# Optimization experiments

Hardware: AMD Instinct MI355X
Metric: run time of the kernel (lower is better)

The kernel has to match this reference:

```python
import jax, jax.numpy as jnp
import numpy as np
from jax import lax

SCORE_THR = 0.1
IOU_THR = 0.3
NUM_CLASSES = 80
MAX_COORD = 4096.0  # class offset for class-aware NMS (boxes live in [0, ~1100])


def setup_inputs() -> dict:
    key = jax.random.key(0)
    bs, n = 4, 4096
    k1, k2, k3, k4 = jax.random.split(key, 4)
    # realistic boxes: centers in [0,1024], w/h in [10,210]
    cxcy = jax.random.uniform(k1, (bs, n, 2), minval=0.0, maxval=1024.0)
    wh = jax.random.uniform(k2, (bs, n, 2), minval=10.0, maxval=210.0)
    x1y1 = cxcy - wh * 0.5
    x2y2 = cxcy + wh * 0.5
    scores = jax.random.uniform(k3, (bs, n, 1), minval=0.0, maxval=1.0)
    cls = jax.random.randint(k4, (bs, n, 1), 0, NUM_CLASSES).astype(jnp.float32)
    batch_preds = jnp.concatenate([x1y1, x2y2, scores, cls], axis=-1)  # [bs, n, 6]
    return {"batch_preds": batch_preds}


def _iou_matrix(boxes):
    # boxes: [N, 4] (x1, y1, x2, y2) -> pairwise IoU [N, N]
    x1, y1, x2, y2 = boxes[:, 0], boxes[:, 1], boxes[:, 2], boxes[:, 3]
    area = (x2 - x1) * (y2 - y1)
    ix1 = jnp.maximum(x1[:, None], x1[None, :])
    iy1 = jnp.maximum(y1[:, None], y1[None, :])
    ix2 = jnp.minimum(x2[:, None], x2[None, :])
    iy2 = jnp.minimum(y2[:, None], y2[None, :])
    inter = jnp.maximum(ix2 - ix1, 0.0) * jnp.maximum(iy2 - iy1, 0.0)
    return inter / (area[:, None] + area[None, :] - inter + 1e-9)


def _nms_image(preds):
    # preds: [N, 6]. Returns preds zeroed where not kept (fixed-shape mask NMS).
    n = preds.shape[0]
    boxes, scores, cls = preds[:, :4], preds[:, 4], preds[:, 5]
    valid = scores >= SCORE_THR
    # class-aware trick == per-class NMS: offset boxes by class so cross-class IoU = 0
    obox = boxes + (cls * MAX_COORD)[:, None]
    order = jnp.argsort(-jnp.where(valid, scores, -jnp.inf))
    sboxes = obox[order]
    svalid = valid[order]
    iou = _iou_matrix(sboxes)  # [N, N]
    idxs = jnp.arange(n)

    def body(suppressed, inp):
        iou_row, v_i, i = inp
        keep_i = v_i & jnp.logical_not(suppressed[i])
        suppressed = suppressed | (keep_i & (iou_row > IOU_THR) & (idxs > i))
        return suppressed, keep_i

    _, keep_sorted = lax.scan(body, jnp.zeros((n,), bool), (iou, svalid, idxs))
    keep = jnp.zeros((n,), bool).at[order].set(keep_sorted)
    return preds * keep[:, None].astype(preds.dtype)


def reference(batch_preds):
    # Fixed-shape formulation of score filtering + per-class greedy NMS:
    # suppressed / below-threshold rows are zeroed instead of removed.
    return jax.vmap(_nms_image)(batch_preds)
```

## Files before the change

kernel.cpp:

```cpp
#include <hip/hip_runtime.h>
#include <hip/hip_bf16.h>

typedef unsigned long long u64;

#define BS 4
#define NBOX 4096
#define NCLS 80
#define CAPC 128
#define ZBLK 16
#define SCORE_THR 0.1f
#define IOU_THR 0.3f
#define MAX_COORD 4096.0f

__global__ __launch_bounds__(64) void k_nms_all(const float* __restrict__ preds,
                                                float* __restrict__ out) {
    const int img = blockIdx.y;
    const int bx = blockIdx.x;
    const int lane = threadIdx.x;
    const float* P = preds + (size_t)img * NBOX * 6;
    float* O = out + (size_t)img * NBOX * 6;

    if (bx >= NCLS) {
        const int base = (bx - NCLS) * (NBOX / ZBLK);
#pragma unroll
        for (int r = 0; r < (NBOX / ZBLK) / 64; ++r) {
            int e = base + lane + r * 64;
            float sc = P[(size_t)e * 6 + 4];
            if (sc < SCORE_THR) {
                float* W = O + (size_t)e * 6;
#pragma unroll
                for (int q = 0; q < 6; ++q) W[q] = 0.0f;
            }
        }
        return;
    }

    __shared__ unsigned mem[CAPC];
    __shared__ unsigned scnt;
    __shared__ u64 skey[CAPC];
    __shared__ float4 sbx[CAPC];
    __shared__ unsigned sidx[CAPC];
    const int cls = bx;
    if (lane == 0) scnt = 0;
    __syncthreads();

    for (int m = lane; m < NBOX; m += 64) {
        float2 sc = *(const float2*)(P + (size_t)m * 6 + 4);
        if (sc.x >= SCORE_THR && (int)sc.y == cls) {
            unsigned slot = atomicAdd(&scnt, 1u);
            if (slot < CAPC) mem[slot] = (unsigned)m;
        }
    }
    __syncthreads();
    const int s = (int)min(scnt, (unsigned)CAPC);
    if (s == 0) return;

    u64 key[2];
    float4 bx2[2] = {make_float4(0,0,0,0), make_float4(0,0,0,0)};
    unsigned oi[2] = {0, 0};
#pragma unroll
    for (int r = 0; r < 2; ++r) {
        int m = lane + 64 * r;
        key[r] = ~0ull;
        if (m < s) {
            unsigned e = mem[m];
            oi[r] = e;
            const float* R = P + (size_t)e * 6;
            float x1 = R[0], y1 = R[1], x2 = R[2], y2 = R[3], sc = R[4], cl = R[5];
            float off = cl * MAX_COORD;
            bx2[r] = make_float4(x1 + off, y1 + off, x2 + off, y2 + off);
            unsigned u = __float_as_uint(sc);
            u = (u & 0x80000000u) ? ~u : (u | 0x80000000u);
            key[r] = ((u64)(~u) << 32) | (u64)e;
        }
        skey[m] = key[r];
    }
    __syncthreads();

    int rank[2] = {0, 0};
    for (int j = 0; j < s; ++j) {
        u64 kj = skey[j];
        rank[0] += (kj < key[0]);
        rank[1] += (kj < key[1]);
    }
    __syncthreads();
#pragma unroll
    for (int r = 0; r < 2; ++r) {
        int m = lane + 64 * r;
        if (m < s) { sbx[rank[r]] = bx2[r]; sidx[rank[r]] = oi[r]; }
    }
    __syncthreads();

    float4 cb[2] = {make_float4(0,0,0,0), make_float4(0,0,0,0)};
    float ca[2] = {0.f, 0.f};
    unsigned coi[2] = {0, 0};
    bool removed[2];
#pragma unroll
    for (int r = 0; r < 2; ++r) {
        int c = lane + 64 * r;
        removed[r] = (c >= s);
        if (c < s) {
            cb[r] = sbx[c];
            coi[r] = sidx[c];
            ca[r] = (cb[r].z - cb[r].x) * (cb[r].w - cb[r].y);
        }
    }

    for (int i = 0; i < s; ++i) {
        u64 mA = __ballot(removed[0]);
        u64 mB = __ballot(removed[1]);
        u64 m = (i < 64) ? mA : mB;
        bool kept = !((m >> (i & 63)) & 1ull);
        if (kept) {
            float4 rb = sbx[i];
            float ra = (rb.z - rb.x) * (rb.w - rb.y);
#pragma unroll
            for (int r = 0; r < 2; ++r) {
                int c = lane + 64 * r;
                if (c > i && !removed[r]) {
                    float ix1 = fmaxf(rb.x, cb[r].x), iy1 = fmaxf(rb.y, cb[r].y);
                    float ix2 = fminf(rb.z, cb[r].z), iy2 = fminf(rb.w, cb[r].w);
                    float iw = fmaxf(ix2 - ix1, 0.f), ih = fmaxf(iy2 - iy1, 0.f);
                    float inter = iw * ih;
                    float iou = inter / (ra + ca[r] - inter + 1e-9f);
                    if (iou > IOU_THR) removed[r] = true;
                }
            }
        }
    }

#pragma unroll
    for (int r = 0; r < 2; ++r) {
        int c = lane + 64 * r;
        if (c < s) {
            unsigned e = coi[r];
            const float* R = P + (size_t)e * 6;
            float* W = O + (size_t)e * 6;
            if (!removed[r]) {
#pragma unroll
                for (int q = 0; q < 6; ++q) W[q] = R[q];
            } else {
#pragma unroll
                for (int q = 0; q < 6; ++q) W[q] = 0.0f;
            }
        }
    }
}

extern "C" void kernel_launch(void* const* d_in, const int* in_sizes, int n_in,
                              void* d_out, int out_size, void* d_ws, size_t ws_size,
                              hipStream_t stream) {
    const float* preds = (const float*)d_in[0];
    float* out = (float*)d_out;
    k_nms_all<<<dim3(NCLS + ZBLK, BS), 64, 0, stream>>>(preds, out);
}
```

Baseline: 90.89 us.

## Widen NMS blocks to four wavefronts for class scan, ranking and writeback

Each block grows from one wavefront to 256 threads. All four waves share the class-membership scan over the 4096 boxes, and up to 128 threads compute sort ranks with one key each. Only wave 0 runs the serial suppression loop, and it publishes the final keep bitmask through shared memory so all threads can do the writeback. The zero-fill blocks drop from 16 to 4 per image, each handling more boxes. The aim is to cut the serial per-block scan and rank latency, at the cost of more threads per block and an extra barrier.

```diff
diff --git a/kernel.cpp b/kernel.cpp
--- a/kernel.cpp
+++ b/kernel.cpp
@@ -7,24 +7,26 @@
 #define NBOX 4096
 #define NCLS 80
 #define CAPC 128
-#define ZBLK 16
+#define ZBLK 4
 #define SCORE_THR 0.1f
 #define IOU_THR 0.3f
 #define MAX_COORD 4096.0f
 
-__global__ __launch_bounds__(64) void k_nms_all(const float* __restrict__ preds,
-                                                float* __restrict__ out) {
+__global__ __launch_bounds__(256) void k_nms_all(const float* __restrict__ preds,
+                                                 float* __restrict__ out) {
     const int img = blockIdx.y;
     const int bx = blockIdx.x;
-    const int lane = threadIdx.x;
+    const int t = threadIdx.x;
+    const int w = t >> 6;
+    const int lane = t & 63;
     const float* P = preds + (size_t)img * NBOX * 6;
     float* O = out + (size_t)img * NBOX * 6;
 
     if (bx >= NCLS) {
         const int base = (bx - NCLS) * (NBOX / ZBLK);
 #pragma unroll
-        for (int r = 0; r < (NBOX / ZBLK) / 64; ++r) {
-            int e = base + lane + r * 64;
+        for (int r = 0; r < (NBOX / ZBLK) / 256; ++r) {
+            int e = base + t + r * 256;
             float sc = P[(size_t)e * 6 + 4];
             if (sc < SCORE_THR) {
                 float* W = O + (size_t)e * 6;
@@ -38,13 +40,14 @@
     __shared__ unsigned mem[CAPC];
     __shared__ unsigned scnt;
     __shared__ u64 skey[CAPC];
-    __shared__ float4 sbx[CAPC];
-    __shared__ unsigned sidx[CAPC];
+    __shared__ float4 sbxs[CAPC];
+    __shared__ unsigned sidxs[CAPC];
+    __shared__ u64 kbm[2];
     const int cls = bx;
-    if (lane == 0) scnt = 0;
+    if (t == 0) scnt = 0;
     __syncthreads();
 
-    for (int m = lane; m < NBOX; m += 64) {
+    for (int m = t; m < NBOX; m += 256) {
         float2 sc = *(const float2*)(P + (size_t)m * 6 + 4);
         if (sc.x >= SCORE_THR && (int)sc.y == cls) {
             unsigned slot = atomicAdd(&scnt, 1u);
@@ -55,94 +58,87 @@
     const int s = (int)min(scnt, (unsigned)CAPC);
     if (s == 0) return;
 
-    u64 key[2];
-    float4 bx2[2] = {make_float4(0,0,0,0), make_float4(0,0,0,0)};
-    unsigned oi[2] = {0, 0};
-#pragma unroll
-    for (int r = 0; r < 2; ++r) {
-        int m = lane + 64 * r;
-        key[r] = ~0ull;
-        if (m < s) {
-            unsigned e = mem[m];
-            oi[r] = e;
+    u64 key = ~0ull;
+    float4 bxv = make_float4(0.f, 0.f, 0.f, 0.f);
+    unsigned oi = 0;
+    if (t < CAPC) {
+        if (t < s) {
+            unsigned e = mem[t];
+            oi = e;
             const float* R = P + (size_t)e * 6;
             float x1 = R[0], y1 = R[1], x2 = R[2], y2 = R[3], sc = R[4], cl = R[5];
             float off = cl * MAX_COORD;
-            bx2[r] = make_float4(x1 + off, y1 + off, x2 + off, y2 + off);
+            bxv = make_float4(x1 + off, y1 + off, x2 + off, y2 + off);
             unsigned u = __float_as_uint(sc);
             u = (u & 0x80000000u) ? ~u : (u | 0x80000000u);
-            key[r] = ((u64)(~u) << 32) | (u64)e;
+            key = ((u64)(~u) << 32) | (u64)e;
         }
-        skey[m] = key[r];
+        skey[t] = key;
     }
     __syncthreads();
 
-    int rank[2] = {0, 0};
-    for (int j = 0; j < s; ++j) {
-        u64 kj = skey[j];
-        rank[0] += (kj < key[0]);
-        rank[1] += (kj < key[1]);
-    }
-    __syncthreads();
-#pragma unroll
-    for (int r = 0; r < 2; ++r) {
-        int m = lane + 64 * r;
-        if (m < s) { sbx[rank[r]] = bx2[r]; sidx[rank[r]] = oi[r]; }
+    if (t < s) {
+        int rank = 0;
+        for (int j = 0; j < s; ++j) rank += (skey[j] < key);
+        sbxs[rank] = bxv;
+        sidxs[rank] = oi;
     }
     __syncthreads();
 
-    float4 cb[2] = {make_float4(0,0,0,0), make_float4(0,0,0,0)};
-    float ca[2] = {0.f, 0.f};
-    unsigned coi[2] = {0, 0};
-    bool removed[2];
+    if (w == 0) {
+        float4 cb[2];
+        float ca[2];
+        bool removed[2];
 #pragma unroll
-    for (int r = 0; r < 2; ++r) {
-        int c = lane + 64 * r;
-        removed[r] = (c >= s);
-        if (c < s) {
-            cb[r] = sbx[c];
-            coi[r] = sidx[c];
-            ca[r] = (cb[r].z - cb[r].x) * (cb[r].w - cb[r].y);
+        for (int r = 0; r < 2; ++r) {
+            int c = lane + 64 * r;
+            removed[r] = (c >= s);
+            cb[r] = make_float4(0.f, 0.f, 0.f, 0.f);
+            ca[r] = 0.f;
+            if (c < s) {
+                cb[r] = sbxs[c];
+                ca[r] = (cb[r].z - cb[r].x) * (cb[r].w - cb[r].y);
+            }
         }
-    }
-
-    for (int i = 0; i < s; ++i) {
-        u64 mA = __ballot(removed[0]);
-        u64 mB = __ballot(removed[1]);
-        u64 m = (i < 64) ? mA : mB;
-        bool kept = !((m >> (i & 63)) & 1ull);
-        if (kept) {
-            float4 rb = sbx[i];
-            float ra = (rb.z - rb.x) * (rb.w - rb.y);
+        for (int i = 0; i < s; ++i) {
+            float4 rb = sbxs[i];
+            u64 mA = __ballot(removed[0]);
+            u64 mB = __ballot(removed[1]);
+            u64 m = (i < 64) ? mA : mB;
+            bool kept = !((m >> (i & 63)) & 1ull);
+            if (kept) {
+                float ra = (rb.z - rb.x) * (rb.w - rb.y);
 #pragma unroll
-            for (int r = 0; r < 2; ++r) {
-                int c = lane + 64 * r;
-                if (c > i && !removed[r]) {
-                    float ix1 = fmaxf(rb.x, cb[r].x), iy1 = fmaxf(rb.y, cb[r].y);
-                    float ix2 = fminf(rb.z, cb[r].z), iy2 = fminf(rb.w, cb[r].w);
-                    float iw = fmaxf(ix2 - ix1, 0.f), ih = fmaxf(iy2 - iy1, 0.f);
-                    float inter = iw * ih;
-                    float iou = inter / (ra + ca[r] - inter + 1e-9f);
-                    if (iou > IOU_THR) removed[r] = true;
+                for (int r = 0; r < 2; ++r) {
+                    int c = lane + 64 * r;
+                    if (c > i && !removed[r]) {
+                        float ix1 = fmaxf(rb.x, cb[r].x), iy1 = fmaxf(rb.y, cb[r].y);
+                        float ix2 = fminf(rb.z, cb[r].z), iy2 = fminf(rb.w, cb[r].w);
+                        float iw = fmaxf(ix2 - ix1, 0.f), ih = fmaxf(iy2 - iy1, 0.f);
+                        float inter = iw * ih;
+                        float iou = inter / (ra + ca[r] - inter + 1e-9f);
+                        if (iou > IOU_THR) removed[r] = true;
+                    }
                 }
             }
         }
+        u64 fA = __ballot(removed[0]);
+        u64 fB = __ballot(removed[1]);
+        if (lane == 0) { kbm[0] = fA; kbm[1] = fB; }
     }
+    __syncthreads();
 
+    if (t < s) {
+        bool rem = (kbm[t >> 6] >> (t & 63)) & 1ull;
+        unsigned e = sidxs[t];
+        const float* R = P + (size_t)e * 6;
+        float* W = O + (size_t)e * 6;
+        if (!rem) {
 #pragma unroll
-    for (int r = 0; r < 2; ++r) {
-        int c = lane + 64 * r;
-        if (c < s) {
-            unsigned e = coi[r];
-            const float* R = P + (size_t)e * 6;
-            float* W = O + (size_t)e * 6;
-            if (!removed[r]) {
+            for (int q = 0; q < 6; ++q) W[q] = R[q];
+        } else {
 #pragma unroll
-                for (int q = 0; q < 6; ++q) W[q] = R[q];
-            } else {
-#pragma unroll
-                for (int q = 0; q < 6; ++q) W[q] = 0.0f;
-            }
+            for (int q = 0; q < 6; ++q) W[q] = 0.0f;
         }
     }
 }
@@ -152,5 +148,5 @@
                               hipStream_t stream) {
     const float* preds = (const float*)d_in[0];
     float* out = (float*)d_out;
-    k_nms_all<<<dim3(NCLS + ZBLK, BS), 64, 0, stream>>>(preds, out);
+    k_nms_all<<<dim3(NCLS + ZBLK, BS), 256, 0, stream>>>(preds, out);
 }
```

Result: faster. 76.38 us (-16.0%).

## Pack 16 classes per 1024-thread block, one wave per class

Applied to the files above, without the earlier changes.

Replaces the one-wave-per-class blocks plus separate zeroing blocks with 5 blocks of 1024 threads per image, each wave owning one class. A single cooperative scan of the image buckets boxes into 16 per-class shared lists, and each block zeroes below-threshold rows for its own slice. This cuts the redundant 80x rescans of the whole image and the block count, but makes each block larger with more shared memory and adds block-wide barriers across waves with uneven work.

```diff
diff --git a/kernel.cpp b/kernel.cpp
--- a/kernel.cpp
+++ b/kernel.cpp
@@ -6,54 +6,54 @@
 #define BS 4
 #define NBOX 4096
 #define NCLS 80
+#define CPB 16
+#define NBLK 5
+#define SLICE 820
 #define CAPC 128
-#define ZBLK 16
 #define SCORE_THR 0.1f
 #define IOU_THR 0.3f
 #define MAX_COORD 4096.0f
 
-__global__ __launch_bounds__(64) void k_nms_all(const float* __restrict__ preds,
-                                                float* __restrict__ out) {
+__global__ __launch_bounds__(1024) void k_nms_all(const float* __restrict__ preds,
+                                                  float* __restrict__ out) {
+    __shared__ unsigned mem[CPB][CAPC];
+    __shared__ unsigned scnt[CPB];
+    __shared__ u64 skey[CPB][CAPC];
+    __shared__ float4 sbxs[CPB][CAPC];
+    __shared__ unsigned sidxs[CPB][CAPC];
+
     const int img = blockIdx.y;
-    const int bx = blockIdx.x;
-    const int lane = threadIdx.x;
+    const int g = blockIdx.x;
+    const int t = threadIdx.x;
+    const int w = t >> 6;
+    const int lane = t & 63;
     const float* P = preds + (size_t)img * NBOX * 6;
     float* O = out + (size_t)img * NBOX * 6;
 
-    if (bx >= NCLS) {
-        const int base = (bx - NCLS) * (NBOX / ZBLK);
-#pragma unroll
-        for (int r = 0; r < (NBOX / ZBLK) / 64; ++r) {
-            int e = base + lane + r * 64;
-            float sc = P[(size_t)e * 6 + 4];
-            if (sc < SCORE_THR) {
-                float* W = O + (size_t)e * 6;
-#pragma unroll
-                for (int q = 0; q < 6; ++q) W[q] = 0.0f;
-            }
-        }
-        return;
-    }
-
-    __shared__ unsigned mem[CAPC];
-    __shared__ unsigned scnt;
-    __shared__ u64 skey[CAPC];
-    __shared__ float4 sbx[CAPC];
-    __shared__ unsigned sidx[CAPC];
-    const int cls = bx;
-    if (lane == 0) scnt = 0;
+    if (t < CPB) scnt[t] = 0;
     __syncthreads();
 
-    for (int m = lane; m < NBOX; m += 64) {
+    const int sbeg = g * SLICE;
+    const int send = min(NBOX, sbeg + SLICE);
+#pragma unroll
+    for (int r = 0; r < NBOX / 1024; ++r) {
+        int m = t + r * 1024;
         float2 sc = *(const float2*)(P + (size_t)m * 6 + 4);
-        if (sc.x >= SCORE_THR && (int)sc.y == cls) {
-            unsigned slot = atomicAdd(&scnt, 1u);
-            if (slot < CAPC) mem[slot] = (unsigned)m;
+        if (sc.x >= SCORE_THR) {
+            int lc = (int)sc.y - g * CPB;
+            if (lc >= 0 && lc < CPB) {
+                unsigned slot = atomicAdd(&scnt[lc], 1u);
+                if (slot < CAPC) mem[lc][slot] = (unsigned)m;
+            }
+        } else if (m >= sbeg && m < send) {
+            float* W = O + (size_t)m * 6;
+#pragma unroll
+            for (int q = 0; q < 6; ++q) W[q] = 0.0f;
         }
     }
     __syncthreads();
-    const int s = (int)min(scnt, (unsigned)CAPC);
-    if (s == 0) return;
+
+    const int s = (int)min(scnt[w], (unsigned)CAPC);
 
     u64 key[2];
     float4 bx2[2] = {make_float4(0,0,0,0), make_float4(0,0,0,0)};
@@ -63,7 +63,7 @@
         int m = lane + 64 * r;
         key[r] = ~0ull;
         if (m < s) {
-            unsigned e = mem[m];
+            unsigned e = mem[w][m];
             oi[r] = e;
             const float* R = P + (size_t)e * 6;
             float x1 = R[0], y1 = R[1], x2 = R[2], y2 = R[3], sc = R[4], cl = R[5];
@@ -73,13 +73,13 @@
             u = (u & 0x80000000u) ? ~u : (u | 0x80000000u);
             key[r] = ((u64)(~u) << 32) | (u64)e;
         }
-        skey[m] = key[r];
+        skey[w][m] = key[r];
     }
     __syncthreads();
 
     int rank[2] = {0, 0};
     for (int j = 0; j < s; ++j) {
-        u64 kj = skey[j];
+        u64 kj = skey[w][j];
         rank[0] += (kj < key[0]);
         rank[1] += (kj < key[1]);
     }
@@ -87,32 +87,31 @@
 #pragma unroll
     for (int r = 0; r < 2; ++r) {
         int m = lane + 64 * r;
-        if (m < s) { sbx[rank[r]] = bx2[r]; sidx[rank[r]] = oi[r]; }
+        if (m < s) { sbxs[w][rank[r]] = bx2[r]; sidxs[w][rank[r]] = oi[r]; }
     }
     __syncthreads();
 
-    float4 cb[2] = {make_float4(0,0,0,0), make_float4(0,0,0,0)};
-    float ca[2] = {0.f, 0.f};
-    unsigned coi[2] = {0, 0};
+    float4 cb[2];
+    float ca[2];
     bool removed[2];
 #pragma unroll
     for (int r = 0; r < 2; ++r) {
         int c = lane + 64 * r;
         removed[r] = (c >= s);
+        cb[r] = make_float4(0.f, 0.f, 0.f, 0.f);
+        ca[r] = 0.f;
         if (c < s) {
-            cb[r] = sbx[c];
-            coi[r] = sidx[c];
+            cb[r] = sbxs[w][c];
             ca[r] = (cb[r].z - cb[r].x) * (cb[r].w - cb[r].y);
         }
     }
-
     for (int i = 0; i < s; ++i) {
+        float4 rb = sbxs[w][i];
         u64 mA = __ballot(removed[0]);
         u64 mB = __ballot(removed[1]);
         u64 m = (i < 64) ? mA : mB;
         bool kept = !((m >> (i & 63)) & 1ull);
         if (kept) {
-            float4 rb = sbx[i];
             float ra = (rb.z - rb.x) * (rb.w - rb.y);
 #pragma unroll
             for (int r = 0; r < 2; ++r) {
@@ -133,7 +132,7 @@
     for (int r = 0; r < 2; ++r) {
         int c = lane + 64 * r;
         if (c < s) {
-            unsigned e = coi[r];
+            unsigned e = sidxs[w][c];
             const float* R = P + (size_t)e * 6;
             float* W = O + (size_t)e * 6;
             if (!removed[r]) {
@@ -152,5 +151,5 @@
                               hipStream_t stream) {
     const float* preds = (const float*)d_in[0];
     float* out = (float*)d_out;
-    k_nms_all<<<dim3(NCLS + ZBLK, BS), 64, 0, stream>>>(preds, out);
+    k_nms_all<<<dim3(NBLK, BS), 1024, 0, stream>>>(preds, out);
 }
```

Result: faster. 75.06 us (-17.4%).
